# Kernel optimization log

Hardware: AMD Instinct MI355X
Metric: run time of the kernel (lower is better)

The kernel has to match this reference:

```python
import jax, jax.numpy as jnp
import numpy as np

IN_CH, PATCH, STRIDE, RES, NCLS = 3, 64, 32, 4096, 1000
SPECTRAL_RADIUS = 0.9


def setup_inputs() -> dict:
    key = jax.random.key(0)
    ks = jax.random.split(key, 8)
    x = jax.random.normal(ks[0], (128, IN_CH, 8224), dtype=jnp.float32)
    # Conv1d weights: [out=PATCH, in=IN_CH, k=PATCH]
    fan_in = IN_CH * PATCH
    bound = 1.0 / np.sqrt(fan_in)
    conv_w = jax.random.uniform(ks[1], (PATCH, IN_CH, PATCH), minval=-bound, maxval=bound, dtype=jnp.float32)
    conv_b = jax.random.uniform(ks[2], (PATCH,), minval=-bound, maxval=bound, dtype=jnp.float32)
    # Reservoir weights (uniform(-0.5, 0.5)), spectral-radius normalized
    rng = np.random.default_rng(0)
    Wres = rng.random((RES, RES), dtype=np.float32) - 0.5
    max_eig = np.max(np.abs(np.linalg.eigvals(Wres)))
    Wres = Wres * (SPECTRAL_RADIUS / max_eig)
    W_reservoir = jnp.asarray(Wres, dtype=jnp.float32)
    W_input = jax.random.uniform(ks[3], (RES, PATCH), minval=-0.5, maxval=0.5, dtype=jnp.float32)
    # cls/dist tokens init to zeros (as in torch)
    cls_token = jnp.zeros((1, PATCH), dtype=jnp.float32)
    dist_token = jnp.zeros((1, PATCH), dtype=jnp.float32)
    hb = 1.0 / np.sqrt(RES)
    w_cls = jax.random.uniform(ks[4], (NCLS, RES), minval=-hb, maxval=hb, dtype=jnp.float32)
    b_cls = jax.random.uniform(ks[5], (NCLS,), minval=-hb, maxval=hb, dtype=jnp.float32)
    w_dist = jax.random.uniform(ks[6], (NCLS, RES), minval=-hb, maxval=hb, dtype=jnp.float32)
    b_dist = jax.random.uniform(ks[7], (NCLS,), minval=-hb, maxval=hb, dtype=jnp.float32)
    return {"x": x, "conv_w": conv_w, "conv_b": conv_b, "W_reservoir": W_reservoir,
            "W_input": W_input, "cls_token": cls_token, "dist_token": dist_token,
            "w_cls": w_cls, "b_cls": b_cls, "w_dist": w_dist, "b_dist": b_dist}


def reference(x, conv_w, conv_b, W_reservoir, W_input, cls_token, dist_token,
              w_cls, b_cls, w_dist, b_dist):
    B = x.shape[0]
    # PatchEmbed: conv1d -> [B, PATCH, L]
    feat = jax.lax.conv_general_dilated(
        x, conv_w, window_strides=(STRIDE,), padding='VALID',
        dimension_numbers=('NCH', 'OIH', 'NCH')) + conv_b[None, :, None]
    WinT = W_input.T  # [PATCH, RES]
    us = jnp.transpose(feat, (2, 0, 1))  # [L, B, PATCH]
    h0 = jnp.zeros((B, RES), dtype=x.dtype)

    def step(h, u):
        h = jnp.tanh(h @ W_reservoir + u @ WinT)
        return h, None

    h, _ = jax.lax.scan(step, h0, us)
    cls_tok = jnp.broadcast_to(cls_token, (B, PATCH))
    dist_tok = jnp.broadcast_to(dist_token, (B, PATCH))
    h_cls = jnp.tanh(h @ W_reservoir + cls_tok @ WinT)
    h_dist = jnp.tanh(h @ W_reservoir + dist_tok @ WinT)
    cls_out = h_cls @ w_cls.T + b_cls
    dist_out = h_dist @ w_dist.T + b_dist
    # eval mode: log_softmax of the averaged logits
    return jax.nn.log_softmax((cls_out + dist_out) * 0.5, axis=1)
```

## Files before the change

### kernel.cpp

```cpp
#include <hip/hip_runtime.h>
#include <hip/hip_bf16.h>

#define LSTEPS 256

typedef short  bf16x8_t  __attribute__((ext_vector_type(8)));
typedef float  f32x4_t   __attribute__((ext_vector_type(4)));
typedef unsigned short us4_t __attribute__((ext_vector_type(4)));

static __device__ __forceinline__ unsigned short f2bf(float f) {
  unsigned int u = __float_as_uint(f);
  unsigned int r = (u + 0x7fffu + ((u >> 16) & 1u)) >> 16;
  return (unsigned short)r;
}
static __device__ __forceinline__ float tanh_fast(float x) {
  float e = __expf(2.f * x);
  return 1.f - 2.f / (e + 1.f);
}

__global__ __launch_bounds__(256) void prep_wc_kernel(
    const float* __restrict__ wcls, const float* __restrict__ wdist,
    unsigned short* __restrict__ Wcat)
{
  const int row = blockIdx.x;
  const float* src = nullptr;
  if (row < 1000) src = wcls + (size_t)row * 4096;
  else if (row >= 1024 && row < 2024) src = wdist + (size_t)(row - 1024) * 4096;
  unsigned short* dst = Wcat + (size_t)row * 4096;
  #pragma unroll 4
  for (int r = 0; r < 16; ++r) {
    const int c = r * 256 + threadIdx.x;
    dst[c] = src ? f2bf(src[c]) : (unsigned short)0;
  }
}

__global__ __launch_bounds__(256) void conv_kernel(
    const float* __restrict__ x, const float* __restrict__ w,
    const float* __restrict__ bias, unsigned short* __restrict__ U)
{
  __shared__ float wl[192][64];
  const int b  = blockIdx.x >> 4;
  const int tg = blockIdx.x & 15;
  const int tid = threadIdx.x;
  for (int i = tid; i < 64 * 192; i += 256)
    wl[i % 192][i / 192] = w[i];
  __syncthreads();
  const int wv = tid >> 6, p = tid & 63;
  const float* xb = x + (size_t)b * (3 * 8224);
  const float bp = bias[p];
  for (int tt = 0; tt < 4; ++tt) {
    const int t = tg * 16 + wv * 4 + tt;
    float acc = bp;
    const float* xw = xb + t * 32;
    #pragma unroll
    for (int c = 0; c < 3; ++c)
      #pragma unroll 8
      for (int k = 0; k < 64; ++k)
        acc += xw[c * 8224 + k] * wl[c * 64 + k][p];
    U[((size_t)t * 8 + (p >> 3)) * 1024 + (size_t)b * 8 + (p & 7)] = f2bf(acc);
  }
}

__global__ __launch_bounds__(256) void prep_tok_kernel(
    const float* __restrict__ cls, const float* __restrict__ dist,
    unsigned short* __restrict__ U)
{
  const int i = blockIdx.x * 256 + threadIdx.x;
  const int s = i >> 13, rem = i & 8191;
  const int kg = rem >> 10, e = rem & 7;
  const float* tok = s ? dist : cls;
  U[(size_t)(256 + s) * 8192 + rem] = f2bf(tok[kg * 8 + e]);
}

__global__ __launch_bounds__(512, 2) void reservoir_persistent(
    const float* __restrict__ wres,
    const unsigned short* __restrict__ U,
    const float* __restrict__ winp,
    unsigned short* __restrict__ A0, unsigned short* __restrict__ A1,
    unsigned short* __restrict__ Hcls, unsigned short* __restrict__ Hdist,
    unsigned int* __restrict__ lcnt, unsigned int* __restrict__ gcnt,
    unsigned int* __restrict__ lgo)
{
  extern __shared__ char smem[];
  float* Pl = (float*)smem;
  unsigned short* Wu = (unsigned short*)(smem + 67584);
  char* Wl2 = smem + 71680;

  const int bid  = blockIdx.x;
  const int tid  = threadIdx.x;
  const int w    = tid >> 6;
  const int lane = tid & 63;
  const int q    = lane >> 4;
  const int r    = lane & 15;
  const int cg   = bid >> 1;
  const int bh   = bid & 1;
  const int nbase = cg * 32;
  const int grp  = bid & 7;
  const int l16  = lane * 16;

  bf16x8_t wf[14][2];
  #pragma unroll
  for (int kk = 0; kk < 16; ++kk)
    #pragma unroll
    for (int ct = 0; ct < 2; ++ct) {
      const float* src = wres + (size_t)(w * 512 + kk * 32 + q * 8) * 4096
                              + nbase + ct * 16 + r;
      bf16x8_t f;
      #pragma unroll
      for (int e = 0; e < 8; ++e) f[e] = (short)f2bf(src[(size_t)e * 4096]);
      if (kk < 14) wf[kk][ct] = f;
      else *(bf16x8_t*)(Wl2 + w * 4096 + ((kk - 14) * 2 + ct) * 1024 + l16) = f;
    }
  if (w < 2) {
    #pragma unroll
    for (int ct = 0; ct < 2; ++ct) {
      const float* src = winp + (size_t)(nbase + ct * 16 + r) * 64 + w * 32 + q * 8;
      bf16x8_t f;
      #pragma unroll
      for (int e = 0; e < 8; ++e) f[e] = (short)f2bf(src[e]);
      *(bf16x8_t*)(Wu + ((size_t)(ct * 2 + w) * 64 + lane) * 8) = f;
    }
  }

  const int au = (w * 64 + q) * 128 + bh * 64 + r;
  const int uu = (w * 4 + q) * 128 + bh * 64 + r;

  const int erow = tid >> 3;
  const int cb   = (tid & 7) * 4;
  const size_t awoff = ((size_t)(cg * 4 + (cb >> 3)) * 128 + bh * 64 + erow) * 8 + (cb & 7);
  const size_t hoff  = (size_t)(bh * 64 + erow) * 4096 + nbase + cb;

  unsigned int phase = 0;

#define LD(BUF, KK)                                                          \
  { BUF[0] = Ab[au + (KK) * 512];      BUF[1] = Ab[au + (KK) * 512 + 16];    \
    BUF[2] = Ab[au + (KK) * 512 + 32]; BUF[3] = Ab[au + (KK) * 512 + 48]; }

#define MMc(BUF, KK)                                                         \
  { acc[0][0] = __builtin_amdgcn_mfma_f32_16x16x32_bf16(BUF[0], wf[KK][0], acc[0][0], 0, 0, 0); \
    acc[0][1] = __builtin_amdgcn_mfma_f32_16x16x32_bf16(BUF[0], wf[KK][1], acc[0][1], 0, 0, 0); \
    acc[1][0] = __builtin_amdgcn_mfma_f32_16x16x32_bf16(BUF[1], wf[KK][0], acc[1][0], 0, 0, 0); \
    acc[1][1] = __builtin_amdgcn_mfma_f32_16x16x32_bf16(BUF[1], wf[KK][1], acc[1][1], 0, 0, 0); \
    acc[2][0] = __builtin_amdgcn_mfma_f32_16x16x32_bf16(BUF[2], wf[KK][0], acc[2][0], 0, 0, 0); \
    acc[2][1] = __builtin_amdgcn_mfma_f32_16x16x32_bf16(BUF[2], wf[KK][1], acc[2][1], 0, 0, 0); \
    acc[3][0] = __builtin_amdgcn_mfma_f32_16x16x32_bf16(BUF[3], wf[KK][0], acc[3][0], 0, 0, 0); \
    acc[3][1] = __builtin_amdgcn_mfma_f32_16x16x32_bf16(BUF[3], wf[KK][1], acc[3][1], 0, 0, 0); }

#define MMW(BUF, W0, W1)                                                     \
  { acc[0][0] = __builtin_amdgcn_mfma_f32_16x16x32_bf16(BUF[0], W0, acc[0][0], 0, 0, 0); \
    acc[0][1] = __builtin_amdgcn_mfma_f32_16x16x32_bf16(BUF[0], W1, acc[0][1], 0, 0, 0); \
    acc[1][0] = __builtin_amdgcn_mfma_f32_16x16x32_bf16(BUF[1], W0, acc[1][0], 0, 0, 0); \
    acc[1][1] = __builtin_amdgcn_mfma_f32_16x16x32_bf16(BUF[1], W1, acc[1][1], 0, 0, 0); \
    acc[2][0] = __builtin_amdgcn_mfma_f32_16x16x32_bf16(BUF[2], W0, acc[2][0], 0, 0, 0); \
    acc[2][1] = __builtin_amdgcn_mfma_f32_16x16x32_bf16(BUF[2], W1, acc[2][1], 0, 0, 0); \
    acc[3][0] = __builtin_amdgcn_mfma_f32_16x16x32_bf16(BUF[3], W0, acc[3][0], 0, 0, 0); \
    acc[3][1] = __builtin_amdgcn_mfma_f32_16x16x32_bf16(BUF[3], W1, acc[3][1], 0, 0, 0); }

  #pragma unroll 1
  for (int t = 0; t < LSTEPS + 2; ++t) {
    const unsigned short* Arp = (t <= LSTEPS) ? ((t & 1) ? A1 : A0) : A0;
    unsigned short* Awp = ((t + 1) & 1) ? A1 : A0;
    const bf16x8_t* __restrict__ Ab = (const bf16x8_t*)Arp;
    const bf16x8_t* __restrict__ Ub = (const bf16x8_t*)(U + (size_t)t * 8192);

    f32x4_t acc[4][2];
    #pragma unroll
    for (int m = 0; m < 4; ++m) {
      acc[m][0] = (f32x4_t){0.f, 0.f, 0.f, 0.f};
      acc[m][1] = (f32x4_t){0.f, 0.f, 0.f, 0.f};
    }

    bf16x8_t b0[4], b1[4], b2[4];
    LD(b0, 0); LD(b1, 1); LD(b2, 2);

    MMc(b0, 0);  LD(b0, 3);
    MMc(b1, 1);  LD(b1, 4);
    MMc(b2, 2);  LD(b2, 5);
    MMc(b0, 3);  LD(b0, 6);
    MMc(b1, 4);  LD(b1, 7);
    MMc(b2, 5);  LD(b2, 8);
    MMc(b0, 6);  LD(b0, 9);
    MMc(b1, 7);  LD(b1, 10);
    MMc(b2, 8);  LD(b2, 11);
    MMc(b0, 9);  LD(b0, 12);
    MMc(b1, 10); LD(b1, 13);
    MMc(b2, 11); LD(b2, 14);
    MMc(b0, 12); LD(b0, 15);

    bf16x8_t bu[4];
    if (w < 2) {
      bu[0] = Ub[uu];      bu[1] = Ub[uu + 16];
      bu[2] = Ub[uu + 32]; bu[3] = Ub[uu + 48];
    }
    MMc(b1, 13);
    {
      const char* wl = Wl2 + w * 4096 + l16;
      bf16x8_t w14a = *(const bf16x8_t*)(wl);
      bf16x8_t w14b = *(const bf16x8_t*)(wl + 1024);
      bf16x8_t w15a = *(const bf16x8_t*)(wl + 2048);
      bf16x8_t w15b = *(const bf16x8_t*)(wl + 3072);
      MMW(b2, w14a, w14b);
      MMW(b0, w15a, w15b);
    }
    if (w < 2) {
      bf16x8_t wu0 = *(const bf16x8_t*)(Wu + ((size_t)(0 * 2 + w) * 64 + lane) * 8);
      bf16x8_t wu1 = *(const bf16x8_t*)(Wu + ((size_t)(1 * 2 + w) * 64 + lane) * 8);
      MMW(bu, wu0, wu1);
    }

    __syncthreads();
    #pragma unroll
    for (int rt = 0; rt < 4; ++rt)
      #pragma unroll
      for (int ct = 0; ct < 2; ++ct)
        #pragma unroll
        for (int i = 0; i < 4; ++i)
          Pl[(w * 64 + rt * 16 + q * 4 + i) * 33 + ct * 16 + r] = acc[rt][ct][i];
    __syncthreads();

    {
      float s0 = 0.f, s1 = 0.f, s2 = 0.f, s3 = 0.f;
      #pragma unroll
      for (int wv = 0; wv < 8; ++wv) {
        const float* p = Pl + (wv * 64 + erow) * 33 + cb;
        s0 += p[0]; s1 += p[1]; s2 += p[2]; s3 += p[3];
      }
      us4_t o;
      o[0] = f2bf(tanh_fast(s0));
      o[1] = f2bf(tanh_fast(s1));
      o[2] = f2bf(tanh_fast(s2));
      o[3] = f2bf(tanh_fast(s3));
      if (t < LSTEPS) {
        *(us4_t*)(Awp + awoff) = o;
      } else {
        unsigned short* H = (t == LSTEPS) ? Hcls : Hdist;
        *(us4_t*)(H + hoff) = o;
      }
    }

    phase += 1;
    __syncthreads();
    if (tid == 0) {
      unsigned int prev = __hip_atomic_fetch_add(&lcnt[grp * 32], 1u,
                            __ATOMIC_RELAXED, __HIP_MEMORY_SCOPE_AGENT);
      if (prev == phase * 32u - 1u) {
        __hip_atomic_fetch_add(gcnt, 1u, __ATOMIC_RELEASE, __HIP_MEMORY_SCOPE_AGENT);
        while (__hip_atomic_load(gcnt, __ATOMIC_RELAXED, __HIP_MEMORY_SCOPE_SYSTEM)
               < phase * 8u)
          __builtin_amdgcn_s_sleep(1);
        (void)__hip_atomic_load(gcnt, __ATOMIC_ACQUIRE, __HIP_MEMORY_SCOPE_AGENT);
        __hip_atomic_store(&lgo[grp * 32], phase,
                           __ATOMIC_RELAXED, __HIP_MEMORY_SCOPE_AGENT);
      } else {
        while (__hip_atomic_load(&lgo[grp * 32], __ATOMIC_RELAXED,
                                 __HIP_MEMORY_SCOPE_SYSTEM) < phase)
          __builtin_amdgcn_s_sleep(1);
      }
    }
    __syncthreads();
  }
#undef LD
#undef MMc
#undef MMW
}

__global__ __launch_bounds__(256) void gemm_ksplit(
    const unsigned short* __restrict__ A0, const unsigned short* __restrict__ A1,
    int nsplit, int lda,
    const unsigned short* __restrict__ BT, int ldb,
    float* __restrict__ P, int ntiles, int klen, int klen_last)
{
  __shared__ unsigned short sA[128 * 64];
  __shared__ unsigned short sB[128 * 64];

  const int bid = blockIdx.x;
  const int nt = bid % ntiles;
  const int s  = bid / ntiles;
  const unsigned short* __restrict__ A = (nt < nsplit) ? A0 : A1;
  const int kb0 = s * klen;
  const int KL  = (s == 7) ? klen_last : klen;
  const int nbase = nt * 128;

  const int tid = threadIdx.x;
  const int w = tid >> 6;
  const int lane = tid & 63;
  const int wr = w >> 1, wc = w & 1;

  f32x4_t acc[4][4];
  #pragma unroll
  for (int m = 0; m < 4; ++m)
    #pragma unroll
    for (int n = 0; n < 4; ++n)
      acc[m][n] = (f32x4_t){0.f, 0.f, 0.f, 0.f};

  const int srow = lane >> 3;
  const int slotL = (lane & 7) ^ srow;

  for (int kb = 0; kb < KL; kb += 64) {
    const int kcol = kb0 + kb + slotL * 8;
    #pragma unroll
    for (int qq = 0; qq < 4; ++qq) {
      const int row = 32 * w + 8 * qq + srow;
      __builtin_amdgcn_global_load_lds(
          (const __attribute__((address_space(1))) void*)(A + (size_t)row * lda + kcol),
          (__attribute__((address_space(3))) void*)(&sA[(32 * w + 8 * qq) * 64]),
          16, 0, 0);
      __builtin_amdgcn_global_load_lds(
          (const __attribute__((address_space(1))) void*)(BT + (size_t)(nbase + row) * ldb + kcol),
          (__attribute__((address_space(3))) void*)(&sB[(32 * w + 8 * qq) * 64]),
          16, 0, 0);
    }
    __syncthreads();

    #pragma unroll
    for (int ksub = 0; ksub < 2; ++ksub) {
      bf16x8_t af[4], bfr[4];
      #pragma unroll
      for (int m = 0; m < 4; ++m) {
        const int row = 64 * wr + 16 * m + (lane & 15);
        const int kslot = (ksub * 4 + (lane >> 4)) ^ (row & 7);
        af[m] = *(const bf16x8_t*)(&sA[row * 64 + kslot * 8]);
      }
      #pragma unroll
      for (int n = 0; n < 4; ++n) {
        const int row = 64 * wc + 16 * n + (lane & 15);
        const int kslot = (ksub * 4 + (lane >> 4)) ^ (row & 7);
        bfr[n] = *(const bf16x8_t*)(&sB[row * 64 + kslot * 8]);
      }
      #pragma unroll
      for (int m = 0; m < 4; ++m)
        #pragma unroll
        for (int n = 0; n < 4; ++n)
          acc[m][n] = __builtin_amdgcn_mfma_f32_16x16x32_bf16(af[m], bfr[n], acc[m][n], 0, 0, 0);
    }
    __syncthreads();
  }

  float* __restrict__ Pp = P + (size_t)s * (128 * 4096);
  #pragma unroll
  for (int m = 0; m < 4; ++m) {
    const int rbase = 64 * wr + 16 * m + ((lane >> 4) << 2);
    #pragma unroll
    for (int n = 0; n < 4; ++n) {
      const int col = nbase + 64 * wc + 16 * n + (lane & 15);
      #pragma unroll
      for (int r = 0; r < 4; ++r)
        Pp[(size_t)(rbase + r) * 4096 + col] = acc[m][n][r];
    }
  }
}

__global__ __launch_bounds__(256) void reduce_linear_kernel(
    const float* __restrict__ P, float* __restrict__ logits)
{
  const int e = blockIdx.x * 1024 + threadIdx.x * 4;
  const int b = e >> 11;
  const int n = e & 2047;
  const size_t off = (size_t)b * 4096 + n;
  float4 sum = *(const float4*)(&P[off]);
  #pragma unroll
  for (int s = 1; s < 8; ++s) {
    float4 v = *(const float4*)(&P[(size_t)s * 524288 + off]);
    sum.x += v.x; sum.y += v.y; sum.z += v.z; sum.w += v.w;
  }
  *(float4*)(&logits[e]) = sum;
}

__global__ __launch_bounds__(256) void logsoftmax_kernel(
    const float* __restrict__ logits, const float* __restrict__ bcls,
    const float* __restrict__ bdist, float* __restrict__ out)
{
  __shared__ float v[1000];
  __shared__ float red[256];
  const int b = blockIdx.x;
  const int tid = threadIdx.x;
  float lmax = -1e30f;
  for (int n = tid; n < 1000; n += 256) {
    float val = 0.5f * (logits[(size_t)b * 2048 + n] + bcls[n]
                      + logits[(size_t)b * 2048 + 1024 + n] + bdist[n]);
    v[n] = val;
    lmax = fmaxf(lmax, val);
  }
  red[tid] = lmax; __syncthreads();
  for (int st = 128; st > 0; st >>= 1) {
    if (tid < st) red[tid] = fmaxf(red[tid], red[tid + st]);
    __syncthreads();
  }
  const float mx = red[0];
  __syncthreads();
  float lsum = 0.f;
  for (int n = tid; n < 1000; n += 256) lsum += expf(v[n] - mx);
  red[tid] = lsum; __syncthreads();
  for (int st = 128; st > 0; st >>= 1) {
    if (tid < st) red[tid] += red[tid + st];
    __syncthreads();
  }
  const float lse = logf(red[0]) + mx;
  for (int n = tid; n < 1000; n += 256) out[(size_t)b * 1000 + n] = v[n] - lse;
}

extern "C" void kernel_launch(void* const* d_in, const int* in_sizes, int n_in,
                              void* d_out, int out_size, void* d_ws, size_t ws_size,
                              hipStream_t stream)
{
  (void)in_sizes; (void)n_in; (void)out_size; (void)ws_size;
  const float* x      = (const float*)d_in[0];
  const float* convw  = (const float*)d_in[1];
  const float* convb  = (const float*)d_in[2];
  const float* wres   = (const float*)d_in[3];
  const float* winp   = (const float*)d_in[4];
  const float* clstok = (const float*)d_in[5];
  const float* dsttok = (const float*)d_in[6];
  const float* wcls   = (const float*)d_in[7];
  const float* bcls   = (const float*)d_in[8];
  const float* wdist  = (const float*)d_in[9];
  const float* bdist  = (const float*)d_in[10];
  float* out = (float*)d_out;

  char* ws = (char*)d_ws;
  unsigned short* U     = (unsigned short*)(ws + 0);
  unsigned short* A0    = (unsigned short*)(ws + 4227072);
  unsigned short* A1    = (unsigned short*)(ws + 5275648);
  unsigned short* Hcls  = (unsigned short*)(ws + 6324224);
  unsigned short* Hdist = (unsigned short*)(ws + 7372800);
  unsigned short* Wcat  = (unsigned short*)(ws + 8421376);
  float*          P     = (float*)(ws + 25198592);
  float*          logit = (float*)(ws + 41975808);
  unsigned int*   lcnt  = (unsigned int*)(ws + 43024384);
  unsigned int*   lgo   = (unsigned int*)(ws + 43025408);
  unsigned int*   gcnt  = (unsigned int*)(ws + 43026432);

  hipFuncSetAttribute((const void*)reservoir_persistent,
                      hipFuncAttributeMaxDynamicSharedMemorySize, 104448);

  hipMemsetAsync(A0, 0, 2 * 1048576, stream);
  hipMemsetAsync(lcnt, 0, 4096, stream);

  prep_wc_kernel<<<2048, 256, 0, stream>>>(wcls, wdist, Wcat);
  conv_kernel<<<2048, 256, 0, stream>>>(x, convw, convb, U);
  prep_tok_kernel<<<64, 256, 0, stream>>>(clstok, dsttok, U);

  reservoir_persistent<<<256, 512, 104448, stream>>>(
      wres, U, winp, A0, A1, Hcls, Hdist, lcnt, gcnt, lgo);

  gemm_ksplit<<<128, 256, 0, stream>>>(Hcls, Hdist, 8, 4096, Wcat, 4096, P, 16, 512, 512);
  reduce_linear_kernel<<<256, 256, 0, stream>>>(P, logit);
  logsoftmax_kernel<<<128, 256, 0, stream>>>(logit, bcls, bdist, out);
}
```

Baseline: 2.916 ms.

## Replace grid-wide barrier with per-wave dataflow counters and triple-buffered state

```diff
diff --git a/kernel.cpp b/kernel.cpp
--- a/kernel.cpp
+++ b/kernel.cpp
@@ -76,9 +76,9 @@
     const unsigned short* __restrict__ U,
     const float* __restrict__ winp,
     unsigned short* __restrict__ A0, unsigned short* __restrict__ A1,
+    unsigned short* __restrict__ A2,
     unsigned short* __restrict__ Hcls, unsigned short* __restrict__ Hdist,
-    unsigned int* __restrict__ lcnt, unsigned int* __restrict__ gcnt,
-    unsigned int* __restrict__ lgo)
+    unsigned int* __restrict__ cnt)
 {
   extern __shared__ char smem[];
   float* Pl = (float*)smem;
@@ -94,7 +94,6 @@
   const int cg   = bid >> 1;
   const int bh   = bid & 1;
   const int nbase = cg * 32;
-  const int grp  = bid & 7;
   const int l16  = lane * 16;
 
   bf16x8_t wf[14][2];
@@ -129,7 +128,8 @@
   const size_t awoff = ((size_t)(cg * 4 + (cb >> 3)) * 128 + bh * 64 + erow) * 8 + (cb & 7);
   const size_t hoff  = (size_t)(bh * 64 + erow) * 4096 + nbase + cb;
 
-  unsigned int phase = 0;
+  volatile unsigned int* mycnt = &cnt[(bh * 8 + w) * 32];
+  unsigned int* addcnt = &cnt[(bh * 8 + (cg >> 4)) * 32];
 
 #define LD(BUF, KK)                                                          \
   { BUF[0] = Ab[au + (KK) * 512];      BUF[1] = Ab[au + (KK) * 512 + 16];    \
@@ -157,10 +157,23 @@
 
   #pragma unroll 1
   for (int t = 0; t < LSTEPS + 2; ++t) {
-    const unsigned short* Arp = (t <= LSTEPS) ? ((t & 1) ? A1 : A0) : A0;
-    unsigned short* Awp = ((t + 1) & 1) ? A1 : A0;
+    const int tr  = (t <= LSTEPS) ? (t % 3) : (LSTEPS % 3);
+    const int tw  = (t + 1) % 3;
+    const unsigned short* Arp = (tr == 0) ? A0 : (tr == 1) ? A1 : A2;
+    unsigned short*       Awp = (tw == 0) ? A0 : (tw == 1) ? A1 : A2;
     const bf16x8_t* __restrict__ Ab = (const bf16x8_t*)Arp;
     const bf16x8_t* __restrict__ Ub = (const bf16x8_t*)(U + (size_t)t * 8192);
+
+    if (t > 0) {
+      const unsigned int thr = 16u * (unsigned int)((t < LSTEPS) ? t : LSTEPS);
+      if (lane == 0) {
+        while (__hip_atomic_load(mycnt, __ATOMIC_RELAXED,
+                                 __HIP_MEMORY_SCOPE_SYSTEM) < thr)
+          __builtin_amdgcn_s_sleep(1);
+      }
+      __builtin_amdgcn_fence(__ATOMIC_ACQUIRE, "agent");
+      __builtin_amdgcn_sched_barrier(0);
+    }
 
     f32x4_t acc[4][2];
     #pragma unroll
@@ -237,26 +250,10 @@
       }
     }
 
-    phase += 1;
-    __syncthreads();
-    if (tid == 0) {
-      unsigned int prev = __hip_atomic_fetch_add(&lcnt[grp * 32], 1u,
-                            __ATOMIC_RELAXED, __HIP_MEMORY_SCOPE_AGENT);
-      if (prev == phase * 32u - 1u) {
-        __hip_atomic_fetch_add(gcnt, 1u, __ATOMIC_RELEASE, __HIP_MEMORY_SCOPE_AGENT);
-        while (__hip_atomic_load(gcnt, __ATOMIC_RELAXED, __HIP_MEMORY_SCOPE_SYSTEM)
-               < phase * 8u)
-          __builtin_amdgcn_s_sleep(1);
-        (void)__hip_atomic_load(gcnt, __ATOMIC_ACQUIRE, __HIP_MEMORY_SCOPE_AGENT);
-        __hip_atomic_store(&lgo[grp * 32], phase,
-                           __ATOMIC_RELAXED, __HIP_MEMORY_SCOPE_AGENT);
-      } else {
-        while (__hip_atomic_load(&lgo[grp * 32], __ATOMIC_RELAXED,
-                                 __HIP_MEMORY_SCOPE_SYSTEM) < phase)
-          __builtin_amdgcn_s_sleep(1);
-      }
-    }
-    __syncthreads();
+    __syncthreads();
+    if (tid == 0 && t < LSTEPS)
+      __hip_atomic_fetch_add(addcnt, 1u, __ATOMIC_RELEASE,
+                             __HIP_MEMORY_SCOPE_AGENT);
   }
 #undef LD
 #undef MMc
@@ -426,8 +423,7 @@
   float*          P     = (float*)(ws + 25198592);
   float*          logit = (float*)(ws + 41975808);
   unsigned int*   lcnt  = (unsigned int*)(ws + 43024384);
-  unsigned int*   lgo   = (unsigned int*)(ws + 43025408);
-  unsigned int*   gcnt  = (unsigned int*)(ws + 43026432);
+  unsigned short* A2    = (unsigned short*)(ws + 25198592);
 
   hipFuncSetAttribute((const void*)reservoir_persistent,
                       hipFuncAttributeMaxDynamicSharedMemorySize, 104448);
@@ -440,7 +436,7 @@
   prep_tok_kernel<<<64, 256, 0, stream>>>(clstok, dsttok, U);
 
   reservoir_persistent<<<256, 512, 104448, stream>>>(
-      wres, U, winp, A0, A1, Hcls, Hdist, lcnt, gcnt, lgo);
+      wres, U, winp, A0, A1, A2, Hcls, Hdist, lcnt);
 
   gemm_ksplit<<<128, 256, 0, stream>>>(Hcls, Hdist, 8, 4096, Wcat, 4096, P, 16, 512, 512);
   reduce_linear_kernel<<<256, 256, 0, stream>>>(P, logit);
```

Measured after the change: 8.312 ms. 185% more time.
